# Optimization experiments

Measured on AMD Instinct MI355X. Metric: run time of the kernel, lower is better.

Reference implementation:

```python
import jax, jax.numpy as jnp
import numpy as np

B, T, INPUT_DIM = 32, 256, 512
VQ_DIM = 128
NUM_EMBED = 8192
CODEBOOK_NUM = 1
SPLIT_NUM = 4
FREQ = INPUT_DIM // 2 + 1  # 257


def setup_inputs() -> dict:
    key = jax.random.key(0)
    k1, k2, k3, k4 = jax.random.split(key, 4)
    x = jax.random.normal(k1, (B, T, INPUT_DIM), dtype=jnp.float32)
    # xavier_normal_ on (input_dim, vq_dim): std = sqrt(2/(fan_in+fan_out))
    xav_std = float(np.sqrt(2.0 / (INPUT_DIM + VQ_DIM)))
    projector = jax.random.normal(k2, (INPUT_DIM, VQ_DIM), dtype=jnp.float32) * xav_std
    codebook = jax.random.normal(k3, (CODEBOOK_NUM, NUM_EMBED, VQ_DIM), dtype=jnp.float32)
    random_matrix = jax.random.randint(k4, (FREQ,), 0, SPLIT_NUM, dtype=jnp.int32)
    return {"x": x, "projector": projector, "codebook": codebook,
            "random_matrix": random_matrix}


def reference(x, projector, codebook, random_matrix):
    n = x.shape[-1]
    x_fft = jnp.fft.rfft(x, axis=-1)                              # [B,T,F] complex
    # masks[s, f] = (random_matrix[f] == s); vectorizes the per-split list
    masks = (random_matrix[None, :] == jnp.arange(SPLIT_NUM)[:, None])  # [S,F] bool
    x_sub = x_fft[:, :, None, :] * masks                           # [B,T,S,F]
    x_recon = jnp.fft.irfft(x_sub, n=n, axis=-1)                   # [B,T,S,n]
    feat = jnp.einsum('btns,sd->btnd', x_recon, projector)         # [B,T,S,D]
    feat = feat / jnp.linalg.norm(feat, axis=-1, keepdims=True)
    cb = codebook / jnp.linalg.norm(codebook, axis=-1, keepdims=True)  # [C,M,D]
    sim = jnp.einsum('btnd,cmd->btncm', feat, cb)                  # [B,T,S,C,M]
    return jnp.argmax(sim, axis=-1)                                # [B,T,S,C]
```

## Files before the change

### kernel.cpp

```cpp
#include <hip/hip_runtime.h>
#include <math.h>

#define BT 8192
#define NDIM 512
#define NFREQ 257
#define DDIM 128
#define NEMBED 8192
#define NQ 4
#define ROWS 32768

typedef _Float16 half8 __attribute__((ext_vector_type(8)));
typedef float f32x4 __attribute__((ext_vector_type(4)));

#define SCALE_DN 2.44140625e-4f

__global__ __launch_bounds__(256) void prep_kernel(const float* __restrict__ cb,
                                                   const float* __restrict__ proj,
                                                   const int* __restrict__ rm,
                                                   _Float16* __restrict__ chi,
                                                   _Float16* __restrict__ clo,
                                                   _Float16* __restrict__ Wth,
                                                   _Float16* __restrict__ Wtl) {
    int t = threadIdx.x;
    if (blockIdx.x < 512) {
        __shared__ float tile[16][132];
        __shared__ float rns[16];
        int tileIdx = blockIdx.x;
        int row = t >> 4, seg = t & 15;
        const float* src = cb + ((size_t)tileIdx * 16 + row) * DDIM + seg * 8;
        float4 v0 = *(const float4*)src;
        float4 v1 = *(const float4*)(src + 4);
        *(float4*)&tile[row][seg * 8] = v0;
        *(float4*)&tile[row][seg * 8 + 4] = v1;
        float ss = v0.x * v0.x;
        ss = fmaf(v0.y, v0.y, ss); ss = fmaf(v0.z, v0.z, ss); ss = fmaf(v0.w, v0.w, ss);
        ss = fmaf(v1.x, v1.x, ss); ss = fmaf(v1.y, v1.y, ss);
        ss = fmaf(v1.z, v1.z, ss); ss = fmaf(v1.w, v1.w, ss);
#pragma unroll
        for (int m = 1; m < 16; m <<= 1) ss += __shfl_xor(ss, m);
        if (seg == 0) rns[row] = 1.0f / sqrtf(ss);
        __syncthreads();
        int cr = t & 15, lgq = (t >> 4) & 3, kt = t >> 6;
        int k0 = kt * 32 + lgq * 8;
        float rn = rns[cr];
        half8 oh, ol;
#pragma unroll
        for (int j = 0; j < 8; ++j) {
            float f = tile[cr][k0 + j] * rn;
            _Float16 h = (_Float16)f;
            oh[j] = h;
            ol[j] = (_Float16)((f - (float)h) * 4096.0f);
        }
        size_t dst = (size_t)tileIdx * 2048 + t * 8;
        *(half8*)(chi + dst) = oh;
        *(half8*)(clo + dst) = ol;
    } else {
        __shared__ float ctab[512];
        __shared__ float Ks[512];
        __shared__ int rms[NFREQ];
        int bxp = blockIdx.x - 512;
        int s = bxp & 3, ntp = bxp >> 2;
        int d = t & 127;
        int n0 = ntp * 16 + (t >> 7) * 8;
        for (int i = t; i < 512; i += 256) ctab[i] = cospif((float)i * (1.0f / 256.0f));
        for (int i = t; i < NFREQ; i += 256) rms[i] = rm[i];
        __syncthreads();
        for (int base = t; base < 512; base += 256) {
            float acc = 0.0f;
            for (int f = 0; f < NFREQ; ++f) {
                float w = (f == 0 || f == 256) ? 1.0f : 2.0f;
                float c = w * ctab[(f * base) & 511];
                acc += (rms[f] == s) ? c : 0.0f;
            }
            Ks[base] = acc * (1.0f / 512.0f);
        }
        __syncthreads();
        float acc[8] = {};
        for (int p16 = 0; p16 < 512; p16 += 16) {
            float wv[23];
#pragma unroll
            for (int j2 = 0; j2 < 23; ++j2) wv[j2] = Ks[(p16 - n0 + j2 - 7) & 511];
#pragma unroll
            for (int j = 0; j < 16; ++j) {
                float xp = proj[(p16 + j) * DDIM + d];
#pragma unroll
                for (int i = 0; i < 8; ++i)
                    acc[i] = fmaf(xp, wv[7 + j - i], acc[i]);
            }
        }
        int set = d >> 4, lr = d & 15;
        int itk = n0 >> 5, lg = (n0 >> 3) & 3;
        size_t idx8 = ((size_t)((s * 16 + itk) * 8 + set)) * 64 + lg * 16 + lr;
        half8 oh, ol;
#pragma unroll
        for (int i = 0; i < 8; ++i) {
            float f = acc[i] * 256.0f;
            _Float16 h = (_Float16)f;
            oh[i] = h;
            ol[i] = (_Float16)((f - (float)h) * 4096.0f);
        }
        *(half8*)(Wth + idx8 * 8) = oh;
        *(half8*)(Wtl + idx8 * 8) = ol;
    }
}

__global__ __launch_bounds__(256) void fused_feat(const float* __restrict__ x,
                                                  const _Float16* __restrict__ Wth,
                                                  const _Float16* __restrict__ Wtl,
                                                  _Float16* __restrict__ fhi,
                                                  _Float16* __restrict__ flo) {
    __shared__ float few[4][16][132];

    int t = threadIdx.x;
    int w = t >> 6, lr = t & 15, lg = (t >> 4) & 3;
    int row0 = blockIdx.x * 64;
    int sIdx = blockIdx.y;

    const half8* wh = (const half8*)Wth;
    const half8* wl = (const half8*)Wtl;
    const float* xrow = x + (size_t)(row0 + w * 16 + lr) * NDIM + lg * 8;

    f32x4 c0[8], c1[8];
#pragma unroll
    for (int i = 0; i < 8; ++i) { c0[i] = (f32x4){0.f,0.f,0.f,0.f}; c1[i] = c0[i]; }

    for (int it = 0; it < 16; ++it) {
        float4 f0 = *(const float4*)(xrow + it * 32);
        float4 f1 = *(const float4*)(xrow + it * 32 + 4);
        float fv[8] = {f0.x, f0.y, f0.z, f0.w, f1.x, f1.y, f1.z, f1.w};
        half8 ah, al;
#pragma unroll
        for (int j = 0; j < 8; ++j) {
            _Float16 h = (_Float16)fv[j];
            ah[j] = h;
            al[j] = (_Float16)((fv[j] - (float)h) * 4096.0f);
        }
        size_t wb = ((size_t)(sIdx * 16 + it) * 8) * 64 + lg * 16 + lr;
#pragma unroll
        for (int set = 0; set < 8; ++set) {
            half8 bh = wh[wb + set * 64];
            half8 bl = wl[wb + set * 64];
            c0[set] = __builtin_amdgcn_mfma_f32_16x16x32_f16(ah, bh, c0[set], 0, 0, 0);
            c1[set] = __builtin_amdgcn_mfma_f32_16x16x32_f16(ah, bl, c1[set], 0, 0, 0);
            c1[set] = __builtin_amdgcn_mfma_f32_16x16x32_f16(al, bh, c1[set], 0, 0, 0);
        }
    }

    float ss[4] = {0.f, 0.f, 0.f, 0.f};
    float vv[8][4];
#pragma unroll
    for (int set = 0; set < 8; ++set)
#pragma unroll
        for (int r = 0; r < 4; ++r) {
            float v = fmaf(c1[set][r], SCALE_DN, c0[set][r]);
            vv[set][r] = v;
            ss[r] = fmaf(v, v, ss[r]);
        }
#pragma unroll
    for (int r = 0; r < 4; ++r) {
#pragma unroll
        for (int m = 1; m < 16; m <<= 1) ss[r] += __shfl_xor(ss[r], m);
    }
    float rn[4];
#pragma unroll
    for (int r = 0; r < 4; ++r) rn[r] = rsqrtf(ss[r]);
#pragma unroll
    for (int set = 0; set < 8; ++set)
#pragma unroll
        for (int r = 0; r < 4; ++r)
            few[w][4 * lg + r][set * 16 + lr] = vv[set][r] * rn[r];
    __syncthreads();
    int l = t & 63;
    int rr = l >> 2, q = l & 3;
    size_t btg = (size_t)(row0 + w * 16 + rr);
    size_t dst = (btg * 4 + sIdx) * DDIM + q * 32;
#pragma unroll
    for (int g = 0; g < 4; ++g) {
        half8 oh, ol;
#pragma unroll
        for (int j = 0; j < 8; ++j) {
            float f = few[w][rr][q * 32 + g * 8 + j];
            _Float16 h = (_Float16)f;
            oh[j] = h;
            ol[j] = (_Float16)((f - (float)h) * 4096.0f);
        }
        *(half8*)(fhi + dst + g * 8) = oh;
        *(half8*)(flo + dst + g * 8) = ol;
    }
}

__global__ __launch_bounds__(256, 2) void sim_argmax_part(const _Float16* __restrict__ fhi,
                                                          const _Float16* __restrict__ flo,
                                                          const _Float16* __restrict__ chi,
                                                          const _Float16* __restrict__ clo,
                                                          float* __restrict__ pv,
                                                          int* __restrict__ pi) {
    __shared__ float redv[256][17];
    __shared__ int   redi[256][17];

    int t = threadIdx.x;
    int w = t >> 6, l = t & 63, lr = t & 15, lg = (t >> 4) & 3;
    int row0 = blockIdx.x * 256;
    int q = blockIdx.y;

    half8 ahi[4][4], alo[4][4];
#pragma unroll
    for (int s = 0; s < 4; ++s)
#pragma unroll
        for (int kt = 0; kt < 4; ++kt) {
            size_t off = (size_t)(row0 + w * 64 + s * 16 + lr) * DDIM + kt * 32 + lg * 8;
            ahi[s][kt] = *(const half8*)(fhi + off);
            alo[s][kt] = *(const half8*)(flo + off);
        }

    const half8* cf = (const half8*)chi;
    const half8* cv = (const half8*)clo;
    size_t base = (size_t)(q * (NEMBED / NQ / 16)) * 256 + l;

    half8 bh[4], bl[4];
#pragma unroll
    for (int kt = 0; kt < 4; ++kt) {
        bh[kt] = cf[base + kt * 64];
        bl[kt] = cv[base + kt * 64];
    }

    float best[4][4];
    int btile[4][4];
#pragma unroll
    for (int s = 0; s < 4; ++s)
#pragma unroll
        for (int r = 0; r < 4; ++r) { best[s][r] = -1e30f; btile[s][r] = 0; }

    const int NT = NEMBED / (16 * NQ);
    for (int it = 0; it < NT; ++it) {
        f32x4 a0[4], a1[4];
#pragma unroll
        for (int s = 0; s < 4; ++s) { a0[s] = (f32x4){0.f,0.f,0.f,0.f}; a1[s] = a0[s]; }
        size_t nb = base + (size_t)(it + 1) * 256;
        bool have = (it + 1) < NT;
        __builtin_amdgcn_s_setprio(1);
#pragma unroll
        for (int kt = 0; kt < 4; ++kt) {
#pragma unroll
            for (int s = 0; s < 4; ++s) {
                a0[s] = __builtin_amdgcn_mfma_f32_16x16x32_f16(ahi[s][kt], bh[kt], a0[s], 0, 0, 0);
                a1[s] = __builtin_amdgcn_mfma_f32_16x16x32_f16(ahi[s][kt], bl[kt], a1[s], 0, 0, 0);
                a1[s] = __builtin_amdgcn_mfma_f32_16x16x32_f16(alo[s][kt], bh[kt], a1[s], 0, 0, 0);
            }
            if (have) {
                bh[kt] = cf[nb + kt * 64];
                bl[kt] = cv[nb + kt * 64];
            }
        }
        __builtin_amdgcn_s_setprio(0);
#pragma unroll
        for (int s = 0; s < 4; ++s)
#pragma unroll
            for (int r = 0; r < 4; ++r) {
                float v = fmaf(a1[s][r], SCALE_DN, a0[s][r]);
                if (v > best[s][r]) { best[s][r] = v; btile[s][r] = it; }
            }
    }

#pragma unroll
    for (int s = 0; s < 4; ++s)
#pragma unroll
        for (int r = 0; r < 4; ++r) {
            int row = w * 64 + s * 16 + 4 * lg + r;
            redv[row][lr] = best[s][r];
            redi[row][lr] = q * (NEMBED / NQ) + btile[s][r] * 16 + lr;
        }
    __syncthreads();
    {
        float bv = redv[t][0]; int bi = redi[t][0];
#pragma unroll
        for (int c = 1; c < 16; ++c) {
            float v = redv[t][c]; int ii = redi[t][c];
            if (v > bv || (v == bv && ii < bi)) { bv = v; bi = ii; }
        }
        pv[(size_t)q * ROWS + row0 + t] = bv;
        pi[(size_t)q * ROWS + row0 + t] = bi;
    }
}

__global__ __launch_bounds__(256) void merge_argmax(const float* __restrict__ pv,
                                                    const int* __restrict__ pi,
                                                    int* __restrict__ out) {
    int row = blockIdx.x * 256 + threadIdx.x;
    float bv = pv[row]; int bi = pi[row];
#pragma unroll
    for (int q = 1; q < NQ; ++q) {
        float v = pv[(size_t)q * ROWS + row];
        if (v > bv) { bv = v; bi = pi[(size_t)q * ROWS + row]; }
    }
    out[row] = bi;
}

extern "C" void kernel_launch(void* const* d_in, const int* in_sizes, int n_in,
                              void* d_out, int out_size, void* d_ws, size_t ws_size,
                              hipStream_t stream) {
    const float* x    = (const float*)d_in[0];
    const float* proj = (const float*)d_in[1];
    const float* cb   = (const float*)d_in[2];
    const int*   rm   = (const int*)d_in[3];
    int* out = (int*)d_out;

    char* wsb = (char*)d_ws;
    _Float16* Wth  = (_Float16*)(wsb + 0);
    _Float16* Wtl  = (_Float16*)(wsb + 524288);
    _Float16* chi  = (_Float16*)(wsb + 1048576);
    _Float16* clo  = (_Float16*)(wsb + 3145728);
    _Float16* fhi  = (_Float16*)(wsb + 5242880);
    _Float16* flo  = (_Float16*)(wsb + 13631488);
    float*    pv   = (float*)(wsb + 22020096);
    int*      pi   = (int*)(wsb + 22544384);

    prep_kernel<<<640, 256, 0, stream>>>(cb, proj, rm, chi, clo, Wth, Wtl);
    fused_feat<<<dim3(128, 4), 256, 0, stream>>>(x, Wth, Wtl, fhi, flo);
    sim_argmax_part<<<dim3(ROWS / 256, NQ), 256, 0, stream>>>(fhi, flo, chi, clo, pv, pi);
    merge_argmax<<<ROWS / 256, 256, 0, stream>>>(pv, pi, out);
}
```

Before: 296.7 us.

## Pre-split x to fp16 hi/lo in prep and stage projector weights in LDS

The prep kernel gains a third block range that converts x once into fp16 hi/lo pairs laid out in MFMA fragment order. fused_feat now reads those pre-split operands instead of redoing the conversion for each of the four splits. It runs 512-thread blocks that each cover 256 rows, with every wave handling two 16-row tiles. Weight fragments are double-buffered in shared memory so all waves reuse one load, which cuts redundant global weight reads and conversion work. The cost is an extra 16MB write/read round trip for x, heavier shared memory use per block, and only 128 blocks in the feature grid.

```diff
diff --git a/kernel.cpp b/kernel.cpp
--- a/kernel.cpp
+++ b/kernel.cpp
@@ -17,14 +17,18 @@
 __global__ __launch_bounds__(256) void prep_kernel(const float* __restrict__ cb,
                                                    const float* __restrict__ proj,
                                                    const int* __restrict__ rm,
+                                                   const float* __restrict__ x,
                                                    _Float16* __restrict__ chi,
                                                    _Float16* __restrict__ clo,
                                                    _Float16* __restrict__ Wth,
-                                                   _Float16* __restrict__ Wtl) {
+                                                   _Float16* __restrict__ Wtl,
+                                                   _Float16* __restrict__ xhi,
+                                                   _Float16* __restrict__ xlo) {
+    __shared__ __align__(16) char psm[33088];
     int t = threadIdx.x;
     if (blockIdx.x < 512) {
-        __shared__ float tile[16][132];
-        __shared__ float rns[16];
+        float (*tile)[132] = (float(*)[132])psm;
+        float* rns = (float*)(psm + 16 * 132 * 4);
         int tileIdx = blockIdx.x;
         int row = t >> 4, seg = t & 15;
         const float* src = cb + ((size_t)tileIdx * 16 + row) * DDIM + seg * 8;
@@ -54,10 +58,10 @@
         size_t dst = (size_t)tileIdx * 2048 + t * 8;
         *(half8*)(chi + dst) = oh;
         *(half8*)(clo + dst) = ol;
-    } else {
-        __shared__ float ctab[512];
-        __shared__ float Ks[512];
-        __shared__ int rms[NFREQ];
+    } else if (blockIdx.x < 640) {
+        float* ctab = (float*)psm;
+        float* Ks   = (float*)(psm + 2048);
+        int*   rms  = (int*)(psm + 4096);
         int bxp = blockIdx.x - 512;
         int s = bxp & 3, ntp = bxp >> 2;
         int d = t & 127;
@@ -101,91 +105,143 @@
         }
         *(half8*)(Wth + idx8 * 8) = oh;
         *(half8*)(Wtl + idx8 * 8) = ol;
-    }
-}
-
-__global__ __launch_bounds__(256) void fused_feat(const float* __restrict__ x,
+    } else {
+        float* xs = (float*)psm;
+        int rt = blockIdx.x - 640;
+        const float* src = x + (size_t)rt * 16 * NDIM;
+#pragma unroll
+        for (int k2 = 0; k2 < 8; ++k2) {
+            int idx = t * 4 + k2 * 1024;
+            float4 v = *(const float4*)(src + idx);
+            *(float4*)&xs[(idx >> 9) * 516 + (idx & 511)] = v;
+        }
+        __syncthreads();
+#pragma unroll
+        for (int k2 = 0; k2 < 4; ++k2) {
+            int s = t + k2 * 256;
+            int it = s >> 6, lg = (s >> 4) & 3, lr = s & 15;
+            const float* p = &xs[lr * 516 + it * 32 + lg * 8];
+            half8 oh, ol;
+#pragma unroll
+            for (int j = 0; j < 8; ++j) {
+                float f = p[j];
+                _Float16 h = (_Float16)f;
+                oh[j] = h;
+                ol[j] = (_Float16)((f - (float)h) * 4096.0f);
+            }
+            size_t d8 = ((size_t)rt * 1024 + s) * 8;
+            *(half8*)(xhi + d8) = oh;
+            *(half8*)(xlo + d8) = ol;
+        }
+    }
+}
+
+__global__ __launch_bounds__(512) void fused_feat(const _Float16* __restrict__ xhi,
+                                                  const _Float16* __restrict__ xlo,
                                                   const _Float16* __restrict__ Wth,
                                                   const _Float16* __restrict__ Wtl,
                                                   _Float16* __restrict__ fhi,
                                                   _Float16* __restrict__ flo) {
-    __shared__ float few[4][16][132];
+    __shared__ half8 Bh[2][512];
+    __shared__ half8 Bl[2][512];
+    __shared__ float few[8][16][132];
 
     int t = threadIdx.x;
-    int w = t >> 6, lr = t & 15, lg = (t >> 4) & 3;
-    int row0 = blockIdx.x * 64;
+    int w = t >> 6, l = t & 63, lr = t & 15, lg = (t >> 4) & 3;
     int sIdx = blockIdx.y;
-
-    const half8* wh = (const half8*)Wth;
-    const half8* wl = (const half8*)Wtl;
-    const float* xrow = x + (size_t)(row0 + w * 16 + lr) * NDIM + lg * 8;
-
-    f32x4 c0[8], c1[8];
-#pragma unroll
-    for (int i = 0; i < 8; ++i) { c0[i] = (f32x4){0.f,0.f,0.f,0.f}; c1[i] = c0[i]; }
+    int rtg0 = blockIdx.x * 16 + w * 2;
+    int rtg1 = rtg0 + 1;
+
+    const half8* ah8 = (const half8*)xhi;
+    const half8* al8 = (const half8*)xlo;
+    const half8* wh8 = (const half8*)Wth;
+    const half8* wl8 = (const half8*)Wtl;
+    size_t wbase = (size_t)sIdx * 16 * 512;
+
+    f32x4 c0[2][8], c1[2][8];
+#pragma unroll
+    for (int s = 0; s < 2; ++s)
+#pragma unroll
+        for (int i = 0; i < 8; ++i) { c0[s][i] = (f32x4){0.f,0.f,0.f,0.f}; c1[s][i] = c0[s][i]; }
+
+    Bh[0][t] = wh8[wbase + t];
+    Bl[0][t] = wl8[wbase + t];
 
     for (int it = 0; it < 16; ++it) {
-        float4 f0 = *(const float4*)(xrow + it * 32);
-        float4 f1 = *(const float4*)(xrow + it * 32 + 4);
-        float fv[8] = {f0.x, f0.y, f0.z, f0.w, f1.x, f1.y, f1.z, f1.w};
-        half8 ah, al;
-#pragma unroll
-        for (int j = 0; j < 8; ++j) {
-            _Float16 h = (_Float16)fv[j];
-            ah[j] = h;
-            al[j] = (_Float16)((fv[j] - (float)h) * 4096.0f);
-        }
-        size_t wb = ((size_t)(sIdx * 16 + it) * 8) * 64 + lg * 16 + lr;
+        __syncthreads();
+        int buf = it & 1;
+        half8 nh, nl;
+        bool have = (it + 1) < 16;
+        if (have) {
+            nh = wh8[wbase + (size_t)(it + 1) * 512 + t];
+            nl = wl8[wbase + (size_t)(it + 1) * 512 + t];
+        }
+        half8 a0h = ah8[(size_t)rtg0 * 1024 + it * 64 + l];
+        half8 a0l = al8[(size_t)rtg0 * 1024 + it * 64 + l];
+        half8 a1h = ah8[(size_t)rtg1 * 1024 + it * 64 + l];
+        half8 a1l = al8[(size_t)rtg1 * 1024 + it * 64 + l];
 #pragma unroll
         for (int set = 0; set < 8; ++set) {
-            half8 bh = wh[wb + set * 64];
-            half8 bl = wl[wb + set * 64];
-            c0[set] = __builtin_amdgcn_mfma_f32_16x16x32_f16(ah, bh, c0[set], 0, 0, 0);
-            c1[set] = __builtin_amdgcn_mfma_f32_16x16x32_f16(ah, bl, c1[set], 0, 0, 0);
-            c1[set] = __builtin_amdgcn_mfma_f32_16x16x32_f16(al, bh, c1[set], 0, 0, 0);
-        }
-    }
-
-    float ss[4] = {0.f, 0.f, 0.f, 0.f};
-    float vv[8][4];
-#pragma unroll
-    for (int set = 0; set < 8; ++set)
+            half8 bh = Bh[buf][set * 64 + l];
+            half8 bl = Bl[buf][set * 64 + l];
+            c0[0][set] = __builtin_amdgcn_mfma_f32_16x16x32_f16(a0h, bh, c0[0][set], 0, 0, 0);
+            c1[0][set] = __builtin_amdgcn_mfma_f32_16x16x32_f16(a0h, bl, c1[0][set], 0, 0, 0);
+            c1[0][set] = __builtin_amdgcn_mfma_f32_16x16x32_f16(a0l, bh, c1[0][set], 0, 0, 0);
+            c0[1][set] = __builtin_amdgcn_mfma_f32_16x16x32_f16(a1h, bh, c0[1][set], 0, 0, 0);
+            c1[1][set] = __builtin_amdgcn_mfma_f32_16x16x32_f16(a1h, bl, c1[1][set], 0, 0, 0);
+            c1[1][set] = __builtin_amdgcn_mfma_f32_16x16x32_f16(a1l, bh, c1[1][set], 0, 0, 0);
+        }
+        __syncthreads();
+        if (have) {
+            Bh[buf ^ 1][t] = nh;
+            Bl[buf ^ 1][t] = nl;
+        }
+    }
+    __syncthreads();
+
+#pragma unroll
+    for (int srow = 0; srow < 2; ++srow) {
+        float ss[4] = {0.f, 0.f, 0.f, 0.f};
+        float vv[8][4];
+#pragma unroll
+        for (int set = 0; set < 8; ++set)
+#pragma unroll
+            for (int r = 0; r < 4; ++r) {
+                float v = fmaf(c1[srow][set][r], SCALE_DN, c0[srow][set][r]);
+                vv[set][r] = v;
+                ss[r] = fmaf(v, v, ss[r]);
+            }
 #pragma unroll
         for (int r = 0; r < 4; ++r) {
-            float v = fmaf(c1[set][r], SCALE_DN, c0[set][r]);
-            vv[set][r] = v;
-            ss[r] = fmaf(v, v, ss[r]);
-        }
-#pragma unroll
-    for (int r = 0; r < 4; ++r) {
-#pragma unroll
-        for (int m = 1; m < 16; m <<= 1) ss[r] += __shfl_xor(ss[r], m);
-    }
-    float rn[4];
-#pragma unroll
-    for (int r = 0; r < 4; ++r) rn[r] = rsqrtf(ss[r]);
-#pragma unroll
-    for (int set = 0; set < 8; ++set)
-#pragma unroll
-        for (int r = 0; r < 4; ++r)
-            few[w][4 * lg + r][set * 16 + lr] = vv[set][r] * rn[r];
-    __syncthreads();
-    int l = t & 63;
-    int rr = l >> 2, q = l & 3;
-    size_t btg = (size_t)(row0 + w * 16 + rr);
-    size_t dst = (btg * 4 + sIdx) * DDIM + q * 32;
-#pragma unroll
-    for (int g = 0; g < 4; ++g) {
-        half8 oh, ol;
-#pragma unroll
-        for (int j = 0; j < 8; ++j) {
-            float f = few[w][rr][q * 32 + g * 8 + j];
-            _Float16 h = (_Float16)f;
-            oh[j] = h;
-            ol[j] = (_Float16)((f - (float)h) * 4096.0f);
-        }
-        *(half8*)(fhi + dst + g * 8) = oh;
-        *(half8*)(flo + dst + g * 8) = ol;
+#pragma unroll
+            for (int m = 1; m < 16; m <<= 1) ss[r] += __shfl_xor(ss[r], m);
+        }
+        float rn[4];
+#pragma unroll
+        for (int r = 0; r < 4; ++r) rn[r] = rsqrtf(ss[r]);
+#pragma unroll
+        for (int set = 0; set < 8; ++set)
+#pragma unroll
+            for (int r = 0; r < 4; ++r)
+                few[w][4 * lg + r][set * 16 + lr] = vv[set][r] * rn[r];
+        __syncthreads();
+        int rr = l >> 2, qq = l & 3;
+        size_t btg = (size_t)(blockIdx.x * 256 + w * 32 + srow * 16 + rr);
+        size_t dst = (btg * 4 + sIdx) * DDIM + qq * 32;
+#pragma unroll
+        for (int g = 0; g < 4; ++g) {
+            half8 oh, ol;
+#pragma unroll
+            for (int j = 0; j < 8; ++j) {
+                float f = few[w][rr][qq * 32 + g * 8 + j];
+                _Float16 h = (_Float16)f;
+                oh[j] = h;
+                ol[j] = (_Float16)((f - (float)h) * 4096.0f);
+            }
+            *(half8*)(fhi + dst + g * 8) = oh;
+            *(half8*)(flo + dst + g * 8) = ol;
+        }
+        __syncthreads();
     }
 }
 
@@ -314,9 +370,11 @@
     _Float16* flo  = (_Float16*)(wsb + 13631488);
     float*    pv   = (float*)(wsb + 22020096);
     int*      pi   = (int*)(wsb + 22544384);
-
-    prep_kernel<<<640, 256, 0, stream>>>(cb, proj, rm, chi, clo, Wth, Wtl);
-    fused_feat<<<dim3(128, 4), 256, 0, stream>>>(x, Wth, Wtl, fhi, flo);
+    _Float16* xhi  = (_Float16*)(wsb + 23068672);
+    _Float16* xlo  = (_Float16*)(wsb + 31457280);
+
+    prep_kernel<<<1152, 256, 0, stream>>>(cb, proj, rm, x, chi, clo, Wth, Wtl, xhi, xlo);
+    fused_feat<<<dim3(32, 4), 512, 0, stream>>>(xhi, xlo, Wth, Wtl, fhi, flo);
     sim_argmax_part<<<dim3(ROWS / 256, NQ), 256, 0, stream>>>(fhi, flo, chi, clo, pv, pi);
     merge_argmax<<<ROWS / 256, 256, 0, stream>>>(pv, pi, out);
 }
```

Result: faster. 284.3 us (-4.2%).
